# Kernel tuning notes

Measured on AMD Instinct MI355X. Metric: run time of the kernel, lower is better.

The kernel has to match this reference:

```python
import jax, jax.numpy as jnp
import numpy as np

QUALITY = 50

# standard JPEG luminance / chrominance quantization tables
_Y_TABLE = np.array([
    [16, 11, 10, 16, 24, 40, 51, 61],
    [12, 12, 14, 19, 26, 58, 60, 55],
    [14, 13, 16, 24, 40, 57, 69, 56],
    [14, 17, 22, 29, 51, 87, 80, 62],
    [18, 22, 37, 56, 68, 109, 103, 77],
    [24, 35, 55, 64, 81, 104, 113, 92],
    [49, 64, 78, 87, 103, 121, 120, 101],
    [72, 92, 95, 98, 112, 100, 103, 99]], dtype=np.float32)
_C_TABLE = np.full((8, 8), 99., dtype=np.float32)
_C_TABLE[:4, :4] = np.array([[17, 18, 24, 47], [18, 21, 26, 66],
                             [24, 26, 56, 99], [47, 66, 99, 99]], dtype=np.float32)

_i = np.arange(8)
_A = np.cos((2 * _i[:, None] + 1) * _i[None, :] * np.pi / 16).astype(np.float32)
_alpha = np.array([1.0 / np.sqrt(2)] + [1.0] * 7, dtype=np.float32)
_ALPHA2 = np.outer(_alpha, _alpha).astype(np.float32)        # idct pre-scale
_SCALE = (_ALPHA2 * 0.25).astype(np.float32)                 # dct post-scale

_RGB2YCC = np.array([[0.299, 0.587, 0.114],
                     [-0.168736, -0.331264, 0.5],
                     [0.5, -0.418688, -0.081312]], dtype=np.float32)
_SHIFT1 = np.array([0., 128., 128.], dtype=np.float32)
_YCC2RGB = np.array([[1., 0., 1.402],
                     [1., -0.344136, -0.714136],
                     [1., 1.772, 0.]], dtype=np.float32)
_SHIFT2 = np.array([0., -128., -128.], dtype=np.float32)


def _diff_round(x):
    r = jnp.round(x)
    return r + (x - r) ** 3


def _jpeg_channel(ch, table, factor):
    # ch: [B, h, w] -> blockwise DCT / quantize / dequant / IDCT -> [B, h, w]
    b, h, w = ch.shape
    blocks = ch.reshape(b, h // 8, 8, w // 8, 8).transpose(0, 1, 3, 2, 4).reshape(b, -1, 8, 8)
    A = jnp.asarray(_A)
    dct = jnp.asarray(_SCALE) * jnp.einsum('bnxy,xu,yv->bnuv', blocks - 128., A, A)
    qt = jnp.asarray(table) * factor
    q = _diff_round(dct / qt)
    deq = q * qt
    idct = 0.25 * jnp.einsum('bnuv,ux,vy->bnxy', deq * jnp.asarray(_ALPHA2), A, A) + 128.
    return idct.reshape(b, h // 8, w // 8, 8, 8).transpose(0, 1, 3, 2, 4).reshape(b, h, w)


def _diff_jpeg(x, quality):
    # quality -> scaling factor
    q = float(quality)
    factor = (5000. / q if q < 50 else 200. - 2. * q) / 100.
    x = jnp.clip(x, 0., 1.)
    img = jnp.transpose(x, (0, 2, 3, 1)) * 255.                      # [B,H,W,3]
    ycc = img @ jnp.asarray(_RGB2YCC).T + jnp.asarray(_SHIFT1)
    y, cb, cr = ycc[..., 0], ycc[..., 1], ycc[..., 2]
    b, h, w = y.shape
    # 4:2:0 chroma subsampling via 2x2 average pooling
    cb_s = cb.reshape(b, h // 2, 2, w // 2, 2).mean(axis=(2, 4))
    cr_s = cr.reshape(b, h // 2, 2, w // 2, 2).mean(axis=(2, 4))
    y2 = _jpeg_channel(y, _Y_TABLE, factor)
    cb2 = _jpeg_channel(cb_s, _C_TABLE, factor)
    cr2 = _jpeg_channel(cr_s, _C_TABLE, factor)
    cb_u = jnp.repeat(jnp.repeat(cb2, 2, axis=1), 2, axis=2)
    cr_u = jnp.repeat(jnp.repeat(cr2, 2, axis=1), 2, axis=2)
    ycc2 = jnp.stack([y2, cb_u, cr_u], axis=-1)
    rgb = (ycc2 + jnp.asarray(_SHIFT2)) @ jnp.asarray(_YCC2RGB).T
    rgb = jnp.clip(rgb, 0., 255.) / 255.
    out = jnp.transpose(rgb, (0, 3, 1, 2))                           # back to NCHW
    return jnp.clip(out, 0., 1.)


def setup_inputs() -> dict:
    key = jax.random.key(0)
    x = jax.random.uniform(key, (32, 3, 512, 512), dtype=jnp.float32)
    return {"x": x}


def reference(x):
    return _diff_jpeg(x, QUALITY)
```

## Files before the change

kernel.cpp:

```cpp
#include <hip/hip_runtime.h>
#include <math.h>

#define HH 512
#define WW 512
#define YS 132
#define CS 68
#define SG 68

typedef float f2 __attribute__((ext_vector_type(2)));
typedef float f4 __attribute__((ext_vector_type(4)));

static __device__ __forceinline__ f4 vclamp01x255(f4 v) {
    f4 z = 0.f, one = 1.f;
    return __builtin_elementwise_max(__builtin_elementwise_min(v, one), z) * 255.f;
}

__device__ __constant__ float YTAB[64] = {
    16,11,10,16,24,40,51,61,
    12,12,14,19,26,58,60,55,
    14,13,16,24,40,57,69,56,
    14,17,22,29,51,87,80,62,
    18,22,37,56,68,109,103,77,
    24,35,55,64,81,104,113,92,
    49,64,78,87,103,121,120,101,
    72,92,95,98,112,100,103,99};
__device__ __constant__ float CTAB[64] = {
    17,18,24,47,99,99,99,99,
    18,21,26,66,99,99,99,99,
    24,26,56,99,99,99,99,99,
    47,66,99,99,99,99,99,99,
    99,99,99,99,99,99,99,99,
    99,99,99,99,99,99,99,99,
    99,99,99,99,99,99,99,99,
    99,99,99,99,99,99,99,99};

__global__ __launch_bounds__(384) void jpeg_fused(const float* __restrict__ in,
                                                  float* __restrict__ out)
{
#pragma clang fp contract(off)
    __shared__ float Yp[16][YS];
    __shared__ float Cbp[8][CS];
    __shared__ float Crp[8][CS];
    __shared__ float Ab[64];
    __shared__ float QY[64], QC[64];
    __shared__ float Scr[6][8 * SG];

    const int tid  = threadIdx.x;
    const int wid  = tid >> 6;
    const int lane = tid & 63;
    const int g    = lane >> 3;
    const int j    = lane & 7;

    const int bid   = blockIdx.x;
    const int b     = bid >> 7;
    const int strip = (bid >> 2) & 31;
    const int rcol  = bid & 3;
    const int h0    = strip * 16;
    const int w0    = rcol * 128;
    const size_t plane = (size_t)HH * WW;

    if (tid < 64) {
        int x = tid >> 3, u = tid & 7;
        double arg = (double)((2 * x + 1) * u) * 3.14159265358979323846 / 16.0;
        Ab[tid] = (float)cos(arg);
        QY[tid] = YTAB[tid];
        QC[tid] = CTAB[tid];
    }

    if (tid < 256) {
        int rowp = tid >> 5;
        int pc   = (tid & 31) * 4;
        int pr   = rowp * 2;
        size_t base = ((size_t)b * 3 * HH + (size_t)(h0 + pr)) * WW + (w0 + pc);
        f4 r0 = *(const f4*)(in + base);
        f4 r1 = *(const f4*)(in + base + WW);
        f4 g0 = *(const f4*)(in + base + plane);
        f4 g1 = *(const f4*)(in + base + plane + WW);
        f4 b0 = *(const f4*)(in + base + 2 * plane);
        f4 b1 = *(const f4*)(in + base + 2 * plane + WW);
        r0 = vclamp01x255(r0); r1 = vclamp01x255(r1);
        g0 = vclamp01x255(g0); g1 = vclamp01x255(g1);
        b0 = vclamp01x255(b0); b1 = vclamp01x255(b1);
        f4 y0  = ((r0 * 0.299f)     + (g0 * 0.587f))     + (b0 * 0.114f);
        f4 y1  = ((r1 * 0.299f)     + (g1 * 0.587f))     + (b1 * 0.114f);
        f4 cb0 = ((r0 * -0.168736f) + (g0 * -0.331264f)) + (b0 * 0.5f);
        f4 cb1 = ((r1 * -0.168736f) + (g1 * -0.331264f)) + (b1 * 0.5f);
        f4 cr0 = ((r0 * 0.5f)       + (g0 * -0.418688f)) + (b0 * -0.081312f);
        f4 cr1 = ((r1 * 0.5f)       + (g1 * -0.418688f)) + (b1 * -0.081312f);
        cb0 = cb0 + 128.f; cb1 = cb1 + 128.f;
        cr0 = cr0 + 128.f; cr1 = cr1 + 128.f;
        y0 = y0 - 128.f;  y1 = y1 - 128.f;
        *(f4*)&Yp[pr][pc]     = y0;
        *(f4*)&Yp[pr + 1][pc] = y1;
        int qc = (tid & 31) * 2;
        {
            float s01a = cb0.x + cb0.y, s23a = cb1.x + cb1.y;
            float s01b = cb0.z + cb0.w, s23b = cb1.z + cb1.w;
            *(float2*)&Cbp[rowp][qc] =
                make_float2((s01a + s23a) / 4.0f, (s01b + s23b) / 4.0f);
        }
        {
            float s01a = cr0.x + cr0.y, s23a = cr1.x + cr1.y;
            float s01b = cr0.z + cr0.w, s23b = cr1.z + cr1.w;
            *(float2*)&Crp[rowp][qc] =
                make_float2((s01a + s23a) / 4.0f, (s01b + s23b) / 4.0f);
        }
    }
    __syncthreads();

    f2 As2[32];
#pragma unroll
    for (int k = 0; k < 32; ++k) {
        As2[k][0] = __int_as_float(__builtin_amdgcn_readfirstlane(__float_as_int(Ab[2 * k])));
        As2[k][1] = __int_as_float(__builtin_amdgcn_readfirstlane(__float_as_int(Ab[2 * k + 1])));
    }

    const bool isY = (wid < 4);
    float* scr = &Scr[wid][0];

    float X[8];
    if (isY) {
        int blk = wid * 8 + g;
        int by = blk >> 4, bx = blk & 15;
#pragma unroll
        for (int x = 0; x < 8; ++x) X[x] = Yp[by * 8 + x][bx * 8 + j];
    } else {
        const float (*Cp)[CS] = (wid == 4) ? Cbp : Crp;
#pragma unroll
        for (int x = 0; x < 8; ++x) X[x] = Cp[x][g * 8 + j] - 128.f;
    }

    f2 Tv[4];
#pragma unroll
    for (int m = 0; m < 4; ++m) {
        f2 a = {0.f, 0.f};
#pragma unroll
        for (int x = 0; x < 8; ++x) {
            f2 xx = {X[x], X[x]};
            a = __builtin_elementwise_fma(xx, As2[x * 4 + m], a);
        }
        Tv[m] = a;
    }
#pragma unroll
    for (int m = 0; m < 4; ++m) {
        scr[g * SG + (2 * m) * 8 + j]     = Tv[m][0];
        scr[g * SG + (2 * m + 1) * 8 + j] = Tv[m][1];
    }
    float Tt[8];
    {
        float4 a = *(const float4*)&scr[g * SG + j * 8];
        float4 c = *(const float4*)&scr[g * SG + j * 8 + 4];
        Tt[0] = a.x; Tt[1] = a.y; Tt[2] = a.z; Tt[3] = a.w;
        Tt[4] = c.x; Tt[5] = c.y; Tt[6] = c.z; Tt[7] = c.w;
    }

    float R[8];
#pragma unroll
    for (int m = 0; m < 4; ++m) {
        f2 a = {0.f, 0.f};
#pragma unroll
        for (int y = 0; y < 8; ++y) {
            f2 tt = {Tt[y], Tt[y]};
            a = __builtin_elementwise_fma(tt, As2[y * 4 + m], a);
        }
        R[2 * m] = a[0]; R[2 * m + 1] = a[1];
    }

    float qt[8];
    {
        const float* QT = isY ? QY : QC;
        float4 a = *(const float4*)&QT[j * 8];
        float4 c = *(const float4*)&QT[j * 8 + 4];
        qt[0] = a.x; qt[1] = a.y; qt[2] = a.z; qt[3] = a.w;
        qt[4] = c.x; qt[5] = c.y; qt[6] = c.z; qt[7] = c.w;
    }
    const float RC = 0.70710678118654752440f;
    float au = (j == 0) ? RC : 1.0f;
    float G[8];
#pragma unroll
    for (int v = 0; v < 8; ++v) {
        float av    = (v == 0) ? RC : 1.0f;
        float a2    = au * av;
        float scale = a2 * 0.25f;
        float dct   = scale * R[v];
        float xq    = dct / qt[v];
        float rd    = rintf(xq);
        float d     = xq - rd;
        float cube  = (d * d) * d;
        float qq    = rd + cube;
        float deq   = qq * qt[v];
        G[v] = deq * a2;
    }
#pragma unroll
    for (int v = 0; v < 8; ++v) scr[g * SG + v * 8 + j] = G[v];
    float Gt[8];
    {
        float4 a = *(const float4*)&scr[g * SG + j * 8];
        float4 c = *(const float4*)&scr[g * SG + j * 8 + 4];
        Gt[0] = a.x; Gt[1] = a.y; Gt[2] = a.z; Gt[3] = a.w;
        Gt[4] = c.x; Gt[5] = c.y; Gt[6] = c.z; Gt[7] = c.w;
    }

    f2 T2v[4];
#pragma unroll
    for (int m = 0; m < 4; ++m) {
        f2 a = {0.f, 0.f};
#pragma unroll
        for (int u = 0; u < 8; ++u) {
            f2 gg = {Gt[u], Gt[u]};
            a = __builtin_elementwise_fma(gg, As2[u * 4 + m], a);
        }
        T2v[m] = a;
    }
#pragma unroll
    for (int m = 0; m < 4; ++m) {
        scr[g * SG + (2 * m) * 8 + j]     = T2v[m][0];
        scr[g * SG + (2 * m + 1) * 8 + j] = T2v[m][1];
    }
    float T2t[8];
    {
        float4 a = *(const float4*)&scr[g * SG + j * 8];
        float4 c = *(const float4*)&scr[g * SG + j * 8 + 4];
        T2t[0] = a.x; T2t[1] = a.y; T2t[2] = a.z; T2t[3] = a.w;
        T2t[4] = c.x; T2t[5] = c.y; T2t[6] = c.z; T2t[7] = c.w;
    }

    float O[8];
#pragma unroll
    for (int m = 0; m < 4; ++m) {
        f2 a = {0.f, 0.f};
#pragma unroll
        for (int v = 0; v < 8; ++v) {
            f2 tt = {T2t[v], T2t[v]};
            a = __builtin_elementwise_fma(tt, As2[v * 4 + m], a);
        }
        a = (a * 0.25f) + 128.f;
        O[2 * m] = a[0]; O[2 * m + 1] = a[1];
    }

    if (isY) {
        int blk = wid * 8 + g;
        int by = blk >> 4, bx = blk & 15;
        *(float4*)&Yp[by * 8 + j][bx * 8]     = make_float4(O[0], O[1], O[2], O[3]);
        *(float4*)&Yp[by * 8 + j][bx * 8 + 4] = make_float4(O[4], O[5], O[6], O[7]);
    } else {
        float (*Cp)[CS] = (wid == 4) ? Cbp : Crp;
        *(float4*)&Cp[j][g * 8]     = make_float4(O[0], O[1], O[2], O[3]);
        *(float4*)&Cp[j][g * 8 + 4] = make_float4(O[4], O[5], O[6], O[7]);
    }
    __syncthreads();

    if (tid < 256) {
        const float INV255 = 1.0f / 255.0f;
        int rowp = tid >> 5;
        int pc   = (tid & 31) * 4;
        int pr   = rowp * 2;
        int qc   = (tid & 31) * 2;
        f4 ya = *(const f4*)&Yp[pr][pc];
        f4 yb = *(const f4*)&Yp[pr + 1][pc];
        float cb0 = Cbp[rowp][qc]     - 128.f;
        float cb1 = Cbp[rowp][qc + 1] - 128.f;
        float cr0 = Crp[rowp][qc]     - 128.f;
        float cr1 = Crp[rowp][qc + 1] - 128.f;
        f4 cbm = {cb0, cb0, cb1, cb1};
        f4 crm = {cr0, cr0, cr1, cr1};
        f4 z = 0.f, m255 = 255.f;
#pragma unroll
        for (int row = 0; row < 2; ++row) {
            f4 yy = row ? yb : ya;
            f4 rv = yy + (crm * 1.402f);
            f4 gv = (yy + (cbm * -0.344136f)) + (crm * -0.714136f);
            f4 bv = yy + (cbm * 1.772f);
            rv = __builtin_elementwise_max(__builtin_elementwise_min(rv, m255), z) * INV255;
            gv = __builtin_elementwise_max(__builtin_elementwise_min(gv, m255), z) * INV255;
            bv = __builtin_elementwise_max(__builtin_elementwise_min(bv, m255), z) * INV255;
            size_t base = ((size_t)b * 3 * HH + (size_t)(h0 + pr + row)) * WW + (w0 + pc);
            __builtin_nontemporal_store(rv, (f4*)(out + base));
            __builtin_nontemporal_store(gv, (f4*)(out + base + plane));
            __builtin_nontemporal_store(bv, (f4*)(out + base + 2 * plane));
        }
    }
}

extern "C" void kernel_launch(void* const* d_in, const int* in_sizes, int n_in,
                              void* d_out, int out_size, void* d_ws, size_t ws_size,
                              hipStream_t stream)
{
    const float* x = (const float*)d_in[0];
    float* o = (float*)d_out;
    int batch  = in_sizes[0] / (3 * HH * WW);
    int blocks = batch * (HH / 16) * (WW / 128);
    jpeg_fused<<<blocks, 384, 0, stream>>>(x, o);
}
```

Before: 41.23 us.

## Process two column tiles per block with prefetched second tile loads

Each block now handles two adjacent 128-column tiles instead of one, halving the grid. The second tile's global loads are issued before the first tile's DCT compute, so memory latency overlaps with compute. The DCT basis and table setup is amortized over both tiles. Plain __syncthreads is replaced with an inline-asm LDS wait plus s_barrier. The trade-off is fewer blocks in flight and higher register pressure from the held prefetch registers.

```diff
diff --git a/kernel.cpp b/kernel.cpp
--- a/kernel.cpp
+++ b/kernel.cpp
@@ -13,6 +13,10 @@
 static __device__ __forceinline__ f4 vclamp01x255(f4 v) {
     f4 z = 0.f, one = 1.f;
     return __builtin_elementwise_max(__builtin_elementwise_min(v, one), z) * 255.f;
+}
+
+static __device__ __forceinline__ void lds_barrier() {
+    asm volatile("s_waitcnt lgkmcnt(0)\n\ts_barrier" ::: "memory");
 }
 
 __device__ __constant__ float YTAB[64] = {
@@ -52,11 +56,11 @@
     const int j    = lane & 7;
 
     const int bid   = blockIdx.x;
-    const int b     = bid >> 7;
-    const int strip = (bid >> 2) & 31;
-    const int rcol  = bid & 3;
+    const int b     = bid >> 6;
+    const int strip = (bid >> 1) & 31;
+    const int half  = bid & 1;
     const int h0    = strip * 16;
-    const int w0    = rcol * 128;
+    const int w0    = half * 256;
     const size_t plane = (size_t)HH * WW;
 
     if (tid < 64) {
@@ -67,20 +71,30 @@
         QC[tid] = CTAB[tid];
     }
 
-    if (tid < 256) {
-        int rowp = tid >> 5;
-        int pc   = (tid & 31) * 4;
-        int pr   = rowp * 2;
-        size_t base = ((size_t)b * 3 * HH + (size_t)(h0 + pr)) * WW + (w0 + pc);
-        f4 r0 = *(const f4*)(in + base);
-        f4 r1 = *(const f4*)(in + base + WW);
-        f4 g0 = *(const f4*)(in + base + plane);
-        f4 g1 = *(const f4*)(in + base + plane + WW);
-        f4 b0 = *(const f4*)(in + base + 2 * plane);
-        f4 b1 = *(const f4*)(in + base + 2 * plane + WW);
-        r0 = vclamp01x255(r0); r1 = vclamp01x255(r1);
-        g0 = vclamp01x255(g0); g1 = vclamp01x255(g1);
-        b0 = vclamp01x255(b0); b1 = vclamp01x255(b1);
+    const int rowp = tid >> 5;
+    const int pc   = (tid & 31) * 4;
+    const int pr   = rowp * 2;
+    const int qc   = (tid & 31) * 2;
+
+    const bool isY = (wid < 4);
+    float* scr = &Scr[wid][0];
+    f2 As2[32];
+
+    auto loadT = [&](f4* L, int tw) {
+        size_t base = ((size_t)b * 3 * HH + (size_t)(h0 + pr)) * WW + (tw + pc);
+        L[0] = *(const f4*)(in + base);
+        L[1] = *(const f4*)(in + base + WW);
+        L[2] = *(const f4*)(in + base + plane);
+        L[3] = *(const f4*)(in + base + plane + WW);
+        L[4] = *(const f4*)(in + base + 2 * plane);
+        L[5] = *(const f4*)(in + base + 2 * plane + WW);
+    };
+
+    auto stageT = [&](const f4* L) {
+#pragma clang fp contract(off)
+        f4 r0 = vclamp01x255(L[0]), r1 = vclamp01x255(L[1]);
+        f4 g0 = vclamp01x255(L[2]), g1 = vclamp01x255(L[3]);
+        f4 b0 = vclamp01x255(L[4]), b1 = vclamp01x255(L[5]);
         f4 y0  = ((r0 * 0.299f)     + (g0 * 0.587f))     + (b0 * 0.114f);
         f4 y1  = ((r1 * 0.299f)     + (g1 * 0.587f))     + (b1 * 0.114f);
         f4 cb0 = ((r0 * -0.168736f) + (g0 * -0.331264f)) + (b0 * 0.5f);
@@ -92,7 +106,6 @@
         y0 = y0 - 128.f;  y1 = y1 - 128.f;
         *(f4*)&Yp[pr][pc]     = y0;
         *(f4*)&Yp[pr + 1][pc] = y1;
-        int qc = (tid & 31) * 2;
         {
             float s01a = cb0.x + cb0.y, s23a = cb1.x + cb1.y;
             float s01b = cb0.z + cb0.w, s23b = cb1.z + cb1.w;
@@ -105,157 +118,139 @@
             *(float2*)&Crp[rowp][qc] =
                 make_float2((s01a + s23a) / 4.0f, (s01b + s23b) / 4.0f);
         }
-    }
-    __syncthreads();
-
-    f2 As2[32];
-#pragma unroll
-    for (int k = 0; k < 32; ++k) {
-        As2[k][0] = __int_as_float(__builtin_amdgcn_readfirstlane(__float_as_int(Ab[2 * k])));
-        As2[k][1] = __int_as_float(__builtin_amdgcn_readfirstlane(__float_as_int(Ab[2 * k + 1])));
-    }
-
-    const bool isY = (wid < 4);
-    float* scr = &Scr[wid][0];
-
-    float X[8];
-    if (isY) {
-        int blk = wid * 8 + g;
-        int by = blk >> 4, bx = blk & 15;
-#pragma unroll
-        for (int x = 0; x < 8; ++x) X[x] = Yp[by * 8 + x][bx * 8 + j];
-    } else {
-        const float (*Cp)[CS] = (wid == 4) ? Cbp : Crp;
-#pragma unroll
-        for (int x = 0; x < 8; ++x) X[x] = Cp[x][g * 8 + j] - 128.f;
-    }
-
-    f2 Tv[4];
-#pragma unroll
-    for (int m = 0; m < 4; ++m) {
-        f2 a = {0.f, 0.f};
-#pragma unroll
-        for (int x = 0; x < 8; ++x) {
-            f2 xx = {X[x], X[x]};
-            a = __builtin_elementwise_fma(xx, As2[x * 4 + m], a);
-        }
-        Tv[m] = a;
-    }
-#pragma unroll
-    for (int m = 0; m < 4; ++m) {
-        scr[g * SG + (2 * m) * 8 + j]     = Tv[m][0];
-        scr[g * SG + (2 * m + 1) * 8 + j] = Tv[m][1];
-    }
-    float Tt[8];
-    {
-        float4 a = *(const float4*)&scr[g * SG + j * 8];
-        float4 c = *(const float4*)&scr[g * SG + j * 8 + 4];
-        Tt[0] = a.x; Tt[1] = a.y; Tt[2] = a.z; Tt[3] = a.w;
-        Tt[4] = c.x; Tt[5] = c.y; Tt[6] = c.z; Tt[7] = c.w;
-    }
-
-    float R[8];
-#pragma unroll
-    for (int m = 0; m < 4; ++m) {
-        f2 a = {0.f, 0.f};
-#pragma unroll
-        for (int y = 0; y < 8; ++y) {
-            f2 tt = {Tt[y], Tt[y]};
-            a = __builtin_elementwise_fma(tt, As2[y * 4 + m], a);
-        }
-        R[2 * m] = a[0]; R[2 * m + 1] = a[1];
-    }
-
-    float qt[8];
-    {
-        const float* QT = isY ? QY : QC;
-        float4 a = *(const float4*)&QT[j * 8];
-        float4 c = *(const float4*)&QT[j * 8 + 4];
-        qt[0] = a.x; qt[1] = a.y; qt[2] = a.z; qt[3] = a.w;
-        qt[4] = c.x; qt[5] = c.y; qt[6] = c.z; qt[7] = c.w;
-    }
-    const float RC = 0.70710678118654752440f;
-    float au = (j == 0) ? RC : 1.0f;
-    float G[8];
-#pragma unroll
-    for (int v = 0; v < 8; ++v) {
-        float av    = (v == 0) ? RC : 1.0f;
-        float a2    = au * av;
-        float scale = a2 * 0.25f;
-        float dct   = scale * R[v];
-        float xq    = dct / qt[v];
-        float rd    = rintf(xq);
-        float d     = xq - rd;
-        float cube  = (d * d) * d;
-        float qq    = rd + cube;
-        float deq   = qq * qt[v];
-        G[v] = deq * a2;
-    }
-#pragma unroll
-    for (int v = 0; v < 8; ++v) scr[g * SG + v * 8 + j] = G[v];
-    float Gt[8];
-    {
-        float4 a = *(const float4*)&scr[g * SG + j * 8];
-        float4 c = *(const float4*)&scr[g * SG + j * 8 + 4];
-        Gt[0] = a.x; Gt[1] = a.y; Gt[2] = a.z; Gt[3] = a.w;
-        Gt[4] = c.x; Gt[5] = c.y; Gt[6] = c.z; Gt[7] = c.w;
-    }
-
-    f2 T2v[4];
-#pragma unroll
-    for (int m = 0; m < 4; ++m) {
-        f2 a = {0.f, 0.f};
-#pragma unroll
-        for (int u = 0; u < 8; ++u) {
-            f2 gg = {Gt[u], Gt[u]};
-            a = __builtin_elementwise_fma(gg, As2[u * 4 + m], a);
-        }
-        T2v[m] = a;
-    }
-#pragma unroll
-    for (int m = 0; m < 4; ++m) {
-        scr[g * SG + (2 * m) * 8 + j]     = T2v[m][0];
-        scr[g * SG + (2 * m + 1) * 8 + j] = T2v[m][1];
-    }
-    float T2t[8];
-    {
-        float4 a = *(const float4*)&scr[g * SG + j * 8];
-        float4 c = *(const float4*)&scr[g * SG + j * 8 + 4];
-        T2t[0] = a.x; T2t[1] = a.y; T2t[2] = a.z; T2t[3] = a.w;
-        T2t[4] = c.x; T2t[5] = c.y; T2t[6] = c.z; T2t[7] = c.w;
-    }
-
-    float O[8];
-#pragma unroll
-    for (int m = 0; m < 4; ++m) {
-        f2 a = {0.f, 0.f};
+    };
+
+    auto computeT = [&]() {
+#pragma clang fp contract(off)
+        float X[8];
+        if (isY) {
+            int blk = wid * 8 + g;
+            int by = blk >> 4, bx = blk & 15;
+#pragma unroll
+            for (int x = 0; x < 8; ++x) X[x] = Yp[by * 8 + x][bx * 8 + j];
+        } else {
+            const float (*Cp)[CS] = (wid == 4) ? Cbp : Crp;
+#pragma unroll
+            for (int x = 0; x < 8; ++x) X[x] = Cp[x][g * 8 + j] - 128.f;
+        }
+        f2 Tv[4];
+#pragma unroll
+        for (int m = 0; m < 4; ++m) {
+            f2 a = {0.f, 0.f};
+#pragma unroll
+            for (int x = 0; x < 8; ++x) {
+                f2 xx = {X[x], X[x]};
+                a = __builtin_elementwise_fma(xx, As2[x * 4 + m], a);
+            }
+            Tv[m] = a;
+        }
+#pragma unroll
+        for (int m = 0; m < 4; ++m) {
+            scr[g * SG + (2 * m) * 8 + j]     = Tv[m][0];
+            scr[g * SG + (2 * m + 1) * 8 + j] = Tv[m][1];
+        }
+        float Tt[8];
+        {
+            float4 a = *(const float4*)&scr[g * SG + j * 8];
+            float4 c = *(const float4*)&scr[g * SG + j * 8 + 4];
+            Tt[0] = a.x; Tt[1] = a.y; Tt[2] = a.z; Tt[3] = a.w;
+            Tt[4] = c.x; Tt[5] = c.y; Tt[6] = c.z; Tt[7] = c.w;
+        }
+        float R[8];
+#pragma unroll
+        for (int m = 0; m < 4; ++m) {
+            f2 a = {0.f, 0.f};
+#pragma unroll
+            for (int y = 0; y < 8; ++y) {
+                f2 tt = {Tt[y], Tt[y]};
+                a = __builtin_elementwise_fma(tt, As2[y * 4 + m], a);
+            }
+            R[2 * m] = a[0]; R[2 * m + 1] = a[1];
+        }
+        float qt[8];
+        {
+            const float* QT = isY ? QY : QC;
+            float4 a = *(const float4*)&QT[j * 8];
+            float4 c = *(const float4*)&QT[j * 8 + 4];
+            qt[0] = a.x; qt[1] = a.y; qt[2] = a.z; qt[3] = a.w;
+            qt[4] = c.x; qt[5] = c.y; qt[6] = c.z; qt[7] = c.w;
+        }
+        const float RC = 0.70710678118654752440f;
+        float au = (j == 0) ? RC : 1.0f;
+        float G[8];
 #pragma unroll
         for (int v = 0; v < 8; ++v) {
-            f2 tt = {T2t[v], T2t[v]};
-            a = __builtin_elementwise_fma(tt, As2[v * 4 + m], a);
-        }
-        a = (a * 0.25f) + 128.f;
-        O[2 * m] = a[0]; O[2 * m + 1] = a[1];
-    }
-
-    if (isY) {
-        int blk = wid * 8 + g;
-        int by = blk >> 4, bx = blk & 15;
-        *(float4*)&Yp[by * 8 + j][bx * 8]     = make_float4(O[0], O[1], O[2], O[3]);
-        *(float4*)&Yp[by * 8 + j][bx * 8 + 4] = make_float4(O[4], O[5], O[6], O[7]);
-    } else {
-        float (*Cp)[CS] = (wid == 4) ? Cbp : Crp;
-        *(float4*)&Cp[j][g * 8]     = make_float4(O[0], O[1], O[2], O[3]);
-        *(float4*)&Cp[j][g * 8 + 4] = make_float4(O[4], O[5], O[6], O[7]);
-    }
-    __syncthreads();
-
-    if (tid < 256) {
+            float av    = (v == 0) ? RC : 1.0f;
+            float a2    = au * av;
+            float scale = a2 * 0.25f;
+            float dct   = scale * R[v];
+            float xq    = dct / qt[v];
+            float rd    = rintf(xq);
+            float d     = xq - rd;
+            float cube  = (d * d) * d;
+            float qq    = rd + cube;
+            float deq   = qq * qt[v];
+            G[v] = deq * a2;
+        }
+#pragma unroll
+        for (int v = 0; v < 8; ++v) scr[g * SG + v * 8 + j] = G[v];
+        float Gt[8];
+        {
+            float4 a = *(const float4*)&scr[g * SG + j * 8];
+            float4 c = *(const float4*)&scr[g * SG + j * 8 + 4];
+            Gt[0] = a.x; Gt[1] = a.y; Gt[2] = a.z; Gt[3] = a.w;
+            Gt[4] = c.x; Gt[5] = c.y; Gt[6] = c.z; Gt[7] = c.w;
+        }
+        f2 T2v[4];
+#pragma unroll
+        for (int m = 0; m < 4; ++m) {
+            f2 a = {0.f, 0.f};
+#pragma unroll
+            for (int u = 0; u < 8; ++u) {
+                f2 gg = {Gt[u], Gt[u]};
+                a = __builtin_elementwise_fma(gg, As2[u * 4 + m], a);
+            }
+            T2v[m] = a;
+        }
+#pragma unroll
+        for (int m = 0; m < 4; ++m) {
+            scr[g * SG + (2 * m) * 8 + j]     = T2v[m][0];
+            scr[g * SG + (2 * m + 1) * 8 + j] = T2v[m][1];
+        }
+        float T2t[8];
+        {
+            float4 a = *(const float4*)&scr[g * SG + j * 8];
+            float4 c = *(const float4*)&scr[g * SG + j * 8 + 4];
+            T2t[0] = a.x; T2t[1] = a.y; T2t[2] = a.z; T2t[3] = a.w;
+            T2t[4] = c.x; T2t[5] = c.y; T2t[6] = c.z; T2t[7] = c.w;
+        }
+        float O[8];
+#pragma unroll
+        for (int m = 0; m < 4; ++m) {
+            f2 a = {0.f, 0.f};
+#pragma unroll
+            for (int v = 0; v < 8; ++v) {
+                f2 tt = {T2t[v], T2t[v]};
+                a = __builtin_elementwise_fma(tt, As2[v * 4 + m], a);
+            }
+            a = (a * 0.25f) + 128.f;
+            O[2 * m] = a[0]; O[2 * m + 1] = a[1];
+        }
+        if (isY) {
+            int blk = wid * 8 + g;
+            int by = blk >> 4, bx = blk & 15;
+            *(float4*)&Yp[by * 8 + j][bx * 8]     = make_float4(O[0], O[1], O[2], O[3]);
+            *(float4*)&Yp[by * 8 + j][bx * 8 + 4] = make_float4(O[4], O[5], O[6], O[7]);
+        } else {
+            float (*Cp)[CS] = (wid == 4) ? Cbp : Crp;
+            *(float4*)&Cp[j][g * 8]     = make_float4(O[0], O[1], O[2], O[3]);
+            *(float4*)&Cp[j][g * 8 + 4] = make_float4(O[4], O[5], O[6], O[7]);
+        }
+    };
+
+    auto outputT = [&](int tw) {
+#pragma clang fp contract(off)
         const float INV255 = 1.0f / 255.0f;
-        int rowp = tid >> 5;
-        int pc   = (tid & 31) * 4;
-        int pr   = rowp * 2;
-        int qc   = (tid & 31) * 2;
         f4 ya = *(const f4*)&Yp[pr][pc];
         f4 yb = *(const f4*)&Yp[pr + 1][pc];
         float cb0 = Cbp[rowp][qc]     - 128.f;
@@ -274,12 +269,37 @@
             rv = __builtin_elementwise_max(__builtin_elementwise_min(rv, m255), z) * INV255;
             gv = __builtin_elementwise_max(__builtin_elementwise_min(gv, m255), z) * INV255;
             bv = __builtin_elementwise_max(__builtin_elementwise_min(bv, m255), z) * INV255;
-            size_t base = ((size_t)b * 3 * HH + (size_t)(h0 + pr + row)) * WW + (w0 + pc);
+            size_t base = ((size_t)b * 3 * HH + (size_t)(h0 + pr + row)) * WW + (tw + pc);
             __builtin_nontemporal_store(rv, (f4*)(out + base));
             __builtin_nontemporal_store(gv, (f4*)(out + base + plane));
             __builtin_nontemporal_store(bv, (f4*)(out + base + 2 * plane));
         }
+    };
+
+    f4 L0[6], L1[6];
+    if (tid < 256) {
+        loadT(L0, w0);
+        stageT(L0);
+        loadT(L1, w0 + 128);
     }
+    lds_barrier();
+
+#pragma unroll
+    for (int k = 0; k < 32; ++k) {
+        As2[k][0] = __int_as_float(__builtin_amdgcn_readfirstlane(__float_as_int(Ab[2 * k])));
+        As2[k][1] = __int_as_float(__builtin_amdgcn_readfirstlane(__float_as_int(Ab[2 * k + 1])));
+    }
+
+    computeT();
+    lds_barrier();
+    if (tid < 256) {
+        outputT(w0);
+        stageT(L1);
+    }
+    lds_barrier();
+    computeT();
+    lds_barrier();
+    if (tid < 256) outputT(w0 + 128);
 }
 
 extern "C" void kernel_launch(void* const* d_in, const int* in_sizes, int n_in,
@@ -289,6 +309,6 @@
     const float* x = (const float*)d_in[0];
     float* o = (float*)d_out;
     int batch  = in_sizes[0] / (3 * HH * WW);
-    int blocks = batch * (HH / 16) * (WW / 128);
+    int blocks = batch * 32 * 2;
     jpeg_fused<<<blocks, 384, 0, stream>>>(x, o);
 }
```

Measured after the change: 44.21 us. +7.2%, slower.

## Restructure to one 16x16 tile per wavefront, removing block-wide barriers

Applied to the files above, without the earlier changes.

Each wavefront now owns a 16x16 pixel tile: it loads the tile, does color conversion, chroma pooling, the DCT/quantize/IDCT for 4 Y blocks plus 2 chroma blocks, and writes the output entirely inside its own LDS region. This replaces the earlier 384-thread block that needed __syncthreads between stages, with 256-thread blocks of four independent waves that rely only on compiler memory fences. Quant tables are read from constant memory instead of being staged in LDS. In exchange, 2 of 8 lane groups sit idle during the transform, global loads are narrower per lane, and correctness depends on lockstep wave execution with no real barrier.

```diff
diff --git a/kernel.cpp b/kernel.cpp
--- a/kernel.cpp
+++ b/kernel.cpp
@@ -3,12 +3,18 @@
 
 #define HH 512
 #define WW 512
-#define YS 132
-#define CS 68
-#define SG 68
 
 typedef float f2 __attribute__((ext_vector_type(2)));
 typedef float f4 __attribute__((ext_vector_type(4)));
+
+#define OY   0
+#define OCB  320
+#define OCR  416
+#define OCF  512
+#define OCF2 832
+#define OSCR 512
+#define OAB  1152
+#define WSZ  1216
 
 static __device__ __forceinline__ f4 vclamp01x255(f4 v) {
     f4 z = 0.f, one = 1.f;
@@ -34,251 +40,223 @@
     99,99,99,99,99,99,99,99,
     99,99,99,99,99,99,99,99};
 
-__global__ __launch_bounds__(384) void jpeg_fused(const float* __restrict__ in,
+__global__ __launch_bounds__(256) void jpeg_fused(const float* __restrict__ in,
                                                   float* __restrict__ out)
 {
 #pragma clang fp contract(off)
-    __shared__ float Yp[16][YS];
-    __shared__ float Cbp[8][CS];
-    __shared__ float Crp[8][CS];
-    __shared__ float Ab[64];
-    __shared__ float QY[64], QC[64];
-    __shared__ float Scr[6][8 * SG];
+    __shared__ float Wall[4][WSZ];
 
     const int tid  = threadIdx.x;
     const int wid  = tid >> 6;
     const int lane = tid & 63;
-    const int g    = lane >> 3;
-    const int j    = lane & 7;
-
-    const int bid   = blockIdx.x;
-    const int b     = bid >> 7;
-    const int strip = (bid >> 2) & 31;
-    const int rcol  = bid & 3;
-    const int h0    = strip * 16;
-    const int w0    = rcol * 128;
+    float* W = Wall[wid];
+
+    const int t  = blockIdx.x * 4 + wid;
+    const int b  = t >> 10;
+    const int th = (t >> 5) & 31;
+    const int tw = t & 31;
+    const int h0 = th * 16;
+    const int w0 = tw * 16;
     const size_t plane = (size_t)HH * WW;
 
-    if (tid < 64) {
-        int x = tid >> 3, u = tid & 7;
+    const int srow = lane >> 2;
+    const int sc4  = (lane & 3) * 4;
+    const size_t gbase = ((size_t)b * 3 * HH + (size_t)(h0 + srow)) * WW + (w0 + sc4);
+
+    f4 Lr = *(const f4*)(in + gbase);
+    f4 Lg = *(const f4*)(in + gbase + plane);
+    f4 Lb = *(const f4*)(in + gbase + 2 * plane);
+
+    {
+        int x = lane >> 3, u = lane & 7;
         double arg = (double)((2 * x + 1) * u) * 3.14159265358979323846 / 16.0;
-        Ab[tid] = (float)cos(arg);
-        QY[tid] = YTAB[tid];
-        QC[tid] = CTAB[tid];
-    }
-
-    if (tid < 256) {
-        int rowp = tid >> 5;
-        int pc   = (tid & 31) * 4;
-        int pr   = rowp * 2;
-        size_t base = ((size_t)b * 3 * HH + (size_t)(h0 + pr)) * WW + (w0 + pc);
-        f4 r0 = *(const f4*)(in + base);
-        f4 r1 = *(const f4*)(in + base + WW);
-        f4 g0 = *(const f4*)(in + base + plane);
-        f4 g1 = *(const f4*)(in + base + plane + WW);
-        f4 b0 = *(const f4*)(in + base + 2 * plane);
-        f4 b1 = *(const f4*)(in + base + 2 * plane + WW);
-        r0 = vclamp01x255(r0); r1 = vclamp01x255(r1);
-        g0 = vclamp01x255(g0); g1 = vclamp01x255(g1);
-        b0 = vclamp01x255(b0); b1 = vclamp01x255(b1);
-        f4 y0  = ((r0 * 0.299f)     + (g0 * 0.587f))     + (b0 * 0.114f);
-        f4 y1  = ((r1 * 0.299f)     + (g1 * 0.587f))     + (b1 * 0.114f);
-        f4 cb0 = ((r0 * -0.168736f) + (g0 * -0.331264f)) + (b0 * 0.5f);
-        f4 cb1 = ((r1 * -0.168736f) + (g1 * -0.331264f)) + (b1 * 0.5f);
-        f4 cr0 = ((r0 * 0.5f)       + (g0 * -0.418688f)) + (b0 * -0.081312f);
-        f4 cr1 = ((r1 * 0.5f)       + (g1 * -0.418688f)) + (b1 * -0.081312f);
-        cb0 = cb0 + 128.f; cb1 = cb1 + 128.f;
-        cr0 = cr0 + 128.f; cr1 = cr1 + 128.f;
-        y0 = y0 - 128.f;  y1 = y1 - 128.f;
-        *(f4*)&Yp[pr][pc]     = y0;
-        *(f4*)&Yp[pr + 1][pc] = y1;
-        int qc = (tid & 31) * 2;
-        {
-            float s01a = cb0.x + cb0.y, s23a = cb1.x + cb1.y;
-            float s01b = cb0.z + cb0.w, s23b = cb1.z + cb1.w;
-            *(float2*)&Cbp[rowp][qc] =
-                make_float2((s01a + s23a) / 4.0f, (s01b + s23b) / 4.0f);
-        }
-        {
-            float s01a = cr0.x + cr0.y, s23a = cr1.x + cr1.y;
-            float s01b = cr0.z + cr0.w, s23b = cr1.z + cr1.w;
-            *(float2*)&Crp[rowp][qc] =
-                make_float2((s01a + s23a) / 4.0f, (s01b + s23b) / 4.0f);
-        }
-    }
-    __syncthreads();
-
+        W[OAB + lane] = (float)cos(arg);
+    }
     f2 As2[32];
 #pragma unroll
     for (int k = 0; k < 32; ++k) {
-        As2[k][0] = __int_as_float(__builtin_amdgcn_readfirstlane(__float_as_int(Ab[2 * k])));
-        As2[k][1] = __int_as_float(__builtin_amdgcn_readfirstlane(__float_as_int(Ab[2 * k + 1])));
-    }
-
-    const bool isY = (wid < 4);
-    float* scr = &Scr[wid][0];
-
-    float X[8];
-    if (isY) {
-        int blk = wid * 8 + g;
-        int by = blk >> 4, bx = blk & 15;
-#pragma unroll
-        for (int x = 0; x < 8; ++x) X[x] = Yp[by * 8 + x][bx * 8 + j];
-    } else {
-        const float (*Cp)[CS] = (wid == 4) ? Cbp : Crp;
-#pragma unroll
-        for (int x = 0; x < 8; ++x) X[x] = Cp[x][g * 8 + j] - 128.f;
-    }
-
-    f2 Tv[4];
-#pragma unroll
-    for (int m = 0; m < 4; ++m) {
-        f2 a = {0.f, 0.f};
-#pragma unroll
-        for (int x = 0; x < 8; ++x) {
-            f2 xx = {X[x], X[x]};
-            a = __builtin_elementwise_fma(xx, As2[x * 4 + m], a);
-        }
-        Tv[m] = a;
-    }
-#pragma unroll
-    for (int m = 0; m < 4; ++m) {
-        scr[g * SG + (2 * m) * 8 + j]     = Tv[m][0];
-        scr[g * SG + (2 * m + 1) * 8 + j] = Tv[m][1];
-    }
-    float Tt[8];
-    {
-        float4 a = *(const float4*)&scr[g * SG + j * 8];
-        float4 c = *(const float4*)&scr[g * SG + j * 8 + 4];
-        Tt[0] = a.x; Tt[1] = a.y; Tt[2] = a.z; Tt[3] = a.w;
-        Tt[4] = c.x; Tt[5] = c.y; Tt[6] = c.z; Tt[7] = c.w;
-    }
-
-    float R[8];
-#pragma unroll
-    for (int m = 0; m < 4; ++m) {
-        f2 a = {0.f, 0.f};
-#pragma unroll
-        for (int y = 0; y < 8; ++y) {
-            f2 tt = {Tt[y], Tt[y]};
-            a = __builtin_elementwise_fma(tt, As2[y * 4 + m], a);
-        }
-        R[2 * m] = a[0]; R[2 * m + 1] = a[1];
-    }
-
-    float qt[8];
-    {
-        const float* QT = isY ? QY : QC;
-        float4 a = *(const float4*)&QT[j * 8];
-        float4 c = *(const float4*)&QT[j * 8 + 4];
-        qt[0] = a.x; qt[1] = a.y; qt[2] = a.z; qt[3] = a.w;
-        qt[4] = c.x; qt[5] = c.y; qt[6] = c.z; qt[7] = c.w;
-    }
-    const float RC = 0.70710678118654752440f;
-    float au = (j == 0) ? RC : 1.0f;
-    float G[8];
-#pragma unroll
-    for (int v = 0; v < 8; ++v) {
-        float av    = (v == 0) ? RC : 1.0f;
-        float a2    = au * av;
-        float scale = a2 * 0.25f;
-        float dct   = scale * R[v];
-        float xq    = dct / qt[v];
-        float rd    = rintf(xq);
-        float d     = xq - rd;
-        float cube  = (d * d) * d;
-        float qq    = rd + cube;
-        float deq   = qq * qt[v];
-        G[v] = deq * a2;
-    }
-#pragma unroll
-    for (int v = 0; v < 8; ++v) scr[g * SG + v * 8 + j] = G[v];
-    float Gt[8];
-    {
-        float4 a = *(const float4*)&scr[g * SG + j * 8];
-        float4 c = *(const float4*)&scr[g * SG + j * 8 + 4];
-        Gt[0] = a.x; Gt[1] = a.y; Gt[2] = a.z; Gt[3] = a.w;
-        Gt[4] = c.x; Gt[5] = c.y; Gt[6] = c.z; Gt[7] = c.w;
-    }
-
-    f2 T2v[4];
-#pragma unroll
-    for (int m = 0; m < 4; ++m) {
-        f2 a = {0.f, 0.f};
-#pragma unroll
-        for (int u = 0; u < 8; ++u) {
-            f2 gg = {Gt[u], Gt[u]};
-            a = __builtin_elementwise_fma(gg, As2[u * 4 + m], a);
-        }
-        T2v[m] = a;
-    }
-#pragma unroll
-    for (int m = 0; m < 4; ++m) {
-        scr[g * SG + (2 * m) * 8 + j]     = T2v[m][0];
-        scr[g * SG + (2 * m + 1) * 8 + j] = T2v[m][1];
-    }
-    float T2t[8];
-    {
-        float4 a = *(const float4*)&scr[g * SG + j * 8];
-        float4 c = *(const float4*)&scr[g * SG + j * 8 + 4];
-        T2t[0] = a.x; T2t[1] = a.y; T2t[2] = a.z; T2t[3] = a.w;
-        T2t[4] = c.x; T2t[5] = c.y; T2t[6] = c.z; T2t[7] = c.w;
-    }
-
-    float O[8];
-#pragma unroll
-    for (int m = 0; m < 4; ++m) {
-        f2 a = {0.f, 0.f};
+        As2[k][0] = __int_as_float(__builtin_amdgcn_readfirstlane(__float_as_int(W[OAB + 2 * k])));
+        As2[k][1] = __int_as_float(__builtin_amdgcn_readfirstlane(__float_as_int(W[OAB + 2 * k + 1])));
+    }
+
+    {
+        f4 r0 = vclamp01x255(Lr), g0 = vclamp01x255(Lg), b0 = vclamp01x255(Lb);
+        f4 y  = ((r0 * 0.299f)     + (g0 * 0.587f))     + (b0 * 0.114f);
+        f4 cb = ((r0 * -0.168736f) + (g0 * -0.331264f)) + (b0 * 0.5f);
+        f4 cr = ((r0 * 0.5f)       + (g0 * -0.418688f)) + (b0 * -0.081312f);
+        cb = cb + 128.f;
+        cr = cr + 128.f;
+        y  = y - 128.f;
+        *(f4*)&W[OY   + srow * 20 + sc4] = y;
+        *(f4*)&W[OCF  + srow * 20 + sc4] = cb;
+        *(f4*)&W[OCF2 + srow * 20 + sc4] = cr;
+    }
+    asm volatile("" ::: "memory");
+
+    {
+        int cy = lane >> 3, cx = lane & 7;
+        int a0 = OCF + (2 * cy) * 20 + 2 * cx, a1 = a0 + 20;
+        float s01 = W[a0] + W[a0 + 1];
+        float s23 = W[a1] + W[a1 + 1];
+        W[OCB + cy * 12 + cx] = (s01 + s23) / 4.0f;
+        int c0 = OCF2 + (2 * cy) * 20 + 2 * cx, c1 = c0 + 20;
+        float t01 = W[c0] + W[c0 + 1];
+        float t23 = W[c1] + W[c1 + 1];
+        W[OCR + cy * 12 + cx] = (t01 + t23) / 4.0f;
+    }
+    asm volatile("" ::: "memory");
+
+    const int g = lane >> 3, j = lane & 7;
+    if (g < 6) {
+        const bool isY = (g < 4);
+        float* scr = &W[OSCR + g * 68];
+
+        float X[8];
+        if (isY) {
+            int by = g >> 1, bx = g & 1;
+#pragma unroll
+            for (int x = 0; x < 8; ++x) X[x] = W[OY + (by * 8 + x) * 20 + bx * 8 + j];
+        } else {
+            int ob = (g == 4) ? OCB : OCR;
+#pragma unroll
+            for (int x = 0; x < 8; ++x) X[x] = W[ob + x * 12 + j] - 128.f;
+        }
+
+        f2 Tv[4];
+#pragma unroll
+        for (int m = 0; m < 4; ++m) {
+            f2 a = {0.f, 0.f};
+#pragma unroll
+            for (int x = 0; x < 8; ++x) {
+                f2 xx = {X[x], X[x]};
+                a = __builtin_elementwise_fma(xx, As2[x * 4 + m], a);
+            }
+            Tv[m] = a;
+        }
+#pragma unroll
+        for (int m = 0; m < 4; ++m) {
+            scr[(2 * m) * 8 + j]     = Tv[m][0];
+            scr[(2 * m + 1) * 8 + j] = Tv[m][1];
+        }
+        float Tt[8];
+        {
+            float4 a = *(const float4*)&scr[j * 8];
+            float4 c = *(const float4*)&scr[j * 8 + 4];
+            Tt[0] = a.x; Tt[1] = a.y; Tt[2] = a.z; Tt[3] = a.w;
+            Tt[4] = c.x; Tt[5] = c.y; Tt[6] = c.z; Tt[7] = c.w;
+        }
+        float R[8];
+#pragma unroll
+        for (int m = 0; m < 4; ++m) {
+            f2 a = {0.f, 0.f};
+#pragma unroll
+            for (int y = 0; y < 8; ++y) {
+                f2 tt = {Tt[y], Tt[y]};
+                a = __builtin_elementwise_fma(tt, As2[y * 4 + m], a);
+            }
+            R[2 * m] = a[0]; R[2 * m + 1] = a[1];
+        }
+        const float* QT = isY ? YTAB : CTAB;
+        float qt[8];
+        {
+            float4 a = *(const float4*)&QT[j * 8];
+            float4 c = *(const float4*)&QT[j * 8 + 4];
+            qt[0] = a.x; qt[1] = a.y; qt[2] = a.z; qt[3] = a.w;
+            qt[4] = c.x; qt[5] = c.y; qt[6] = c.z; qt[7] = c.w;
+        }
+        const float RC = 0.70710678118654752440f;
+        float au = (j == 0) ? RC : 1.0f;
+        float G[8];
 #pragma unroll
         for (int v = 0; v < 8; ++v) {
-            f2 tt = {T2t[v], T2t[v]};
-            a = __builtin_elementwise_fma(tt, As2[v * 4 + m], a);
-        }
-        a = (a * 0.25f) + 128.f;
-        O[2 * m] = a[0]; O[2 * m + 1] = a[1];
-    }
-
-    if (isY) {
-        int blk = wid * 8 + g;
-        int by = blk >> 4, bx = blk & 15;
-        *(float4*)&Yp[by * 8 + j][bx * 8]     = make_float4(O[0], O[1], O[2], O[3]);
-        *(float4*)&Yp[by * 8 + j][bx * 8 + 4] = make_float4(O[4], O[5], O[6], O[7]);
-    } else {
-        float (*Cp)[CS] = (wid == 4) ? Cbp : Crp;
-        *(float4*)&Cp[j][g * 8]     = make_float4(O[0], O[1], O[2], O[3]);
-        *(float4*)&Cp[j][g * 8 + 4] = make_float4(O[4], O[5], O[6], O[7]);
-    }
-    __syncthreads();
-
-    if (tid < 256) {
+            float av    = (v == 0) ? RC : 1.0f;
+            float a2    = au * av;
+            float scale = a2 * 0.25f;
+            float dct   = scale * R[v];
+            float xq    = dct / qt[v];
+            float rd    = rintf(xq);
+            float d     = xq - rd;
+            float cube  = (d * d) * d;
+            float qq    = rd + cube;
+            float deq   = qq * qt[v];
+            G[v] = deq * a2;
+        }
+#pragma unroll
+        for (int v = 0; v < 8; ++v) scr[v * 8 + j] = G[v];
+        float Gt[8];
+        {
+            float4 a = *(const float4*)&scr[j * 8];
+            float4 c = *(const float4*)&scr[j * 8 + 4];
+            Gt[0] = a.x; Gt[1] = a.y; Gt[2] = a.z; Gt[3] = a.w;
+            Gt[4] = c.x; Gt[5] = c.y; Gt[6] = c.z; Gt[7] = c.w;
+        }
+        f2 T2v[4];
+#pragma unroll
+        for (int m = 0; m < 4; ++m) {
+            f2 a = {0.f, 0.f};
+#pragma unroll
+            for (int u = 0; u < 8; ++u) {
+                f2 gg = {Gt[u], Gt[u]};
+                a = __builtin_elementwise_fma(gg, As2[u * 4 + m], a);
+            }
+            T2v[m] = a;
+        }
+#pragma unroll
+        for (int m = 0; m < 4; ++m) {
+            scr[(2 * m) * 8 + j]     = T2v[m][0];
+            scr[(2 * m + 1) * 8 + j] = T2v[m][1];
+        }
+        float T2t[8];
+        {
+            float4 a = *(const float4*)&scr[j * 8];
+            float4 c = *(const float4*)&scr[j * 8 + 4];
+            T2t[0] = a.x; T2t[1] = a.y; T2t[2] = a.z; T2t[3] = a.w;
+            T2t[4] = c.x; T2t[5] = c.y; T2t[6] = c.z; T2t[7] = c.w;
+        }
+        float O[8];
+#pragma unroll
+        for (int m = 0; m < 4; ++m) {
+            f2 a = {0.f, 0.f};
+#pragma unroll
+            for (int v = 0; v < 8; ++v) {
+                f2 tt = {T2t[v], T2t[v]};
+                a = __builtin_elementwise_fma(tt, As2[v * 4 + m], a);
+            }
+            a = (a * 0.25f) + 128.f;
+            O[2 * m] = a[0]; O[2 * m + 1] = a[1];
+        }
+        if (isY) {
+            int by = g >> 1, bx = g & 1;
+            *(f4*)&W[OY + (by * 8 + j) * 20 + bx * 8]     = (f4){O[0], O[1], O[2], O[3]};
+            *(f4*)&W[OY + (by * 8 + j) * 20 + bx * 8 + 4] = (f4){O[4], O[5], O[6], O[7]};
+        } else {
+            int ob = (g == 4) ? OCB : OCR;
+            *(f4*)&W[ob + j * 12]     = (f4){O[0], O[1], O[2], O[3]};
+            *(f4*)&W[ob + j * 12 + 4] = (f4){O[4], O[5], O[6], O[7]};
+        }
+    }
+    asm volatile("" ::: "memory");
+
+    {
         const float INV255 = 1.0f / 255.0f;
-        int rowp = tid >> 5;
-        int pc   = (tid & 31) * 4;
-        int pr   = rowp * 2;
-        int qc   = (tid & 31) * 2;
-        f4 ya = *(const f4*)&Yp[pr][pc];
-        f4 yb = *(const f4*)&Yp[pr + 1][pc];
-        float cb0 = Cbp[rowp][qc]     - 128.f;
-        float cb1 = Cbp[rowp][qc + 1] - 128.f;
-        float cr0 = Crp[rowp][qc]     - 128.f;
-        float cr1 = Crp[rowp][qc + 1] - 128.f;
+        f4 y2 = *(const f4*)&W[OY + srow * 20 + sc4];
+        int cy = srow >> 1, cc = sc4 >> 1;
+        float cb0 = W[OCB + cy * 12 + cc]     - 128.f;
+        float cb1 = W[OCB + cy * 12 + cc + 1] - 128.f;
+        float cr0 = W[OCR + cy * 12 + cc]     - 128.f;
+        float cr1 = W[OCR + cy * 12 + cc + 1] - 128.f;
         f4 cbm = {cb0, cb0, cb1, cb1};
         f4 crm = {cr0, cr0, cr1, cr1};
         f4 z = 0.f, m255 = 255.f;
-#pragma unroll
-        for (int row = 0; row < 2; ++row) {
-            f4 yy = row ? yb : ya;
-            f4 rv = yy + (crm * 1.402f);
-            f4 gv = (yy + (cbm * -0.344136f)) + (crm * -0.714136f);
-            f4 bv = yy + (cbm * 1.772f);
-            rv = __builtin_elementwise_max(__builtin_elementwise_min(rv, m255), z) * INV255;
-            gv = __builtin_elementwise_max(__builtin_elementwise_min(gv, m255), z) * INV255;
-            bv = __builtin_elementwise_max(__builtin_elementwise_min(bv, m255), z) * INV255;
-            size_t base = ((size_t)b * 3 * HH + (size_t)(h0 + pr + row)) * WW + (w0 + pc);
-            __builtin_nontemporal_store(rv, (f4*)(out + base));
-            __builtin_nontemporal_store(gv, (f4*)(out + base + plane));
-            __builtin_nontemporal_store(bv, (f4*)(out + base + 2 * plane));
-        }
+        f4 rv = y2 + (crm * 1.402f);
+        f4 gv = (y2 + (cbm * -0.344136f)) + (crm * -0.714136f);
+        f4 bv = y2 + (cbm * 1.772f);
+        rv = __builtin_elementwise_max(__builtin_elementwise_min(rv, m255), z) * INV255;
+        gv = __builtin_elementwise_max(__builtin_elementwise_min(gv, m255), z) * INV255;
+        bv = __builtin_elementwise_max(__builtin_elementwise_min(bv, m255), z) * INV255;
+        __builtin_nontemporal_store(rv, (f4*)(out + gbase));
+        __builtin_nontemporal_store(gv, (f4*)(out + gbase + plane));
+        __builtin_nontemporal_store(bv, (f4*)(out + gbase + 2 * plane));
     }
 }
 
@@ -289,6 +267,6 @@
     const float* x = (const float*)d_in[0];
     float* o = (float*)d_out;
     int batch  = in_sizes[0] / (3 * HH * WW);
-    int blocks = batch * (HH / 16) * (WW / 128);
-    jpeg_fused<<<blocks, 384, 0, stream>>>(x, o);
+    int blocks = batch * 1024 / 4;
+    jpeg_fused<<<blocks, 256, 0, stream>>>(x, o);
 }
```

Measured after the change: 45.69 us. +10.8%, slower.
